# Kernel tuning notes

Hardware: AMD Instinct MI355X
Metric: run time of the kernel (lower is better)

## Reference

```python
import jax, jax.numpy as jnp
import numpy as np
from jax import lax

B, T, V, D, K = 64, 512, 32000, 768, 29

def setup_inputs() -> dict:
    key = jax.random.key(0)
    ks = jax.random.split(key, 8)
    x = jax.random.randint(ks[0], (B, T), 0, V)
    tags = jax.random.randint(ks[1], (B, T), 0, K)
    emb = jax.random.normal(ks[2], (V, D), dtype=jnp.float32) * 0.02
    w = jax.random.normal(ks[3], (K, D), dtype=jnp.float32) * 0.02
    b = jnp.zeros((K,), dtype=jnp.float32)
    start_trans = jax.random.normal(ks[4], (K,), dtype=jnp.float32) * 0.1
    end_trans = jax.random.normal(ks[5], (K,), dtype=jnp.float32) * 0.1
    trans = jax.random.normal(ks[6], (K, K), dtype=jnp.float32) * 0.1
    return {"x": x, "tags": tags, "emb": emb, "w": w, "b": b,
            "start_trans": start_trans, "end_trans": end_trans, "trans": trans}

def _emissions(x, emb, w, b):
    e = emb[x]                                   # [B,T,D] (dropout is identity at inference)
    return jnp.einsum('btd,kd->btk', e, w) + b   # [B,T,K]

def _crf_nll(em, tags, start_trans, end_trans, trans):
    # numerator: score of the gold tag path (full mask)
    num = start_trans[tags[:, 0]]
    num = num + jnp.take_along_axis(em[:, 0], tags[:, 0:1], axis=1)[:, 0]
    num = num + jnp.sum(trans[tags[:, :-1], tags[:, 1:]], axis=1)
    num = num + jnp.sum(jnp.take_along_axis(em[:, 1:], tags[:, 1:, None], axis=2)[..., 0], axis=1)
    num = num + end_trans[tags[:, -1]]
    # denominator: forward algorithm (log partition)
    def step(alpha, e_t):
        # alpha [B,K] prev-tag scores; e_t [B,K] current emissions
        nxt = jax.nn.logsumexp(alpha[:, :, None] + trans[None], axis=1) + e_t
        return nxt, None
    alpha0 = start_trans[None] + em[:, 0]
    alpha, _ = lax.scan(step, alpha0, jnp.swapaxes(em[:, 1:], 0, 1))
    logZ = jax.nn.logsumexp(alpha + end_trans[None], axis=1)
    return -jnp.sum(num - logZ)  # torchcrf default reduction='sum', model negates

def _viterbi(em, start_trans, end_trans, trans):
    def vstep(score, e_t):
        cand = score[:, :, None] + trans[None]   # [B,K_prev,K_cur]
        bp = jnp.argmax(cand, axis=1)            # [B,K]
        return jnp.max(cand, axis=1) + e_t, bp
    score0 = start_trans[None] + em[:, 0]
    score, bps = lax.scan(vstep, score0, jnp.swapaxes(em[:, 1:], 0, 1))  # bps [T-1,B,K]
    last = jnp.argmax(score + end_trans[None], axis=1)                   # [B]
    def back(tag, bp):
        prev = jnp.take_along_axis(bp, tag[:, None], axis=1)[:, 0]
        return prev, prev
    _, path = lax.scan(back, last, bps, reverse=True)                    # [T-1,B], tags 0..T-2
    return jnp.concatenate([jnp.swapaxes(path, 0, 1), last[:, None]], axis=1)

def reference(x, tags, emb, w, b, start_trans, end_trans, trans):
    em = _emissions(x, emb, w, b)
    nll = _crf_nll(em, tags, start_trans, end_trans, trans)
    decoded = _viterbi(em, start_trans, end_trans, trans)
    return nll, decoded
```

## Files before the change

kernel.cpp:

```cpp
#include <hip/hip_runtime.h>
#include <math.h>

#define NB 64
#define NT 512
#define ND 768
#define NK 29
#define L2E 1.4426950408889634f
#define LN2 0.6931471805599453f
#define NEG_BIG -1e30f

typedef __attribute__((ext_vector_type(8))) short short8;
typedef __attribute__((ext_vector_type(4))) float floatx4;

__device__ __forceinline__ short bf16r(float f) {
    unsigned u = __float_as_uint(f);
    unsigned r = (u + 0x7FFFu + ((u >> 16) & 1u)) >> 16;
    return (short)r;
}

__global__ __launch_bounds__(256) void k_prep(const float* __restrict__ w,
                                              short* __restrict__ wbf)
{
    int i = blockIdx.x * 256 + threadIdx.x;
    if (i < 32 * ND) {
        int row = i / ND;
        wbf[i] = (row < NK) ? bf16r(w[i]) : (short)0;
    }
}

__global__ __launch_bounds__(128, 2) void k_emissions(
    const int* __restrict__ x, const float* __restrict__ emb,
    const short* __restrict__ wbf, const float* __restrict__ bias,
    float* __restrict__ em)
{
    __shared__ float red[2 * 256];
    const int lane = threadIdx.x & 63;
    const int wv = threadIdx.x >> 6;
    const int col = lane & 15;
    const int quad = lane >> 4;
    const int Mbase = blockIdx.x * 16;
    const int tok = Mbase + col;

    const float* arow = emb + (size_t)x[tok] * ND + wv * 384 + quad * 8;
    const short* brow0 = wbf + (size_t)col * ND + wv * 384 + quad * 8;
    const short* brow1 = brow0 + 16 * ND;

    float4 a[24];
#pragma unroll
    for (int c = 0; c < 12; ++c) {
        a[2 * c]     = *(const float4*)(arow + c * 32);
        a[2 * c + 1] = *(const float4*)(arow + c * 32 + 4);
    }

    floatx4 acc0 = {0.f, 0.f, 0.f, 0.f};
    floatx4 acc1 = {0.f, 0.f, 0.f, 0.f};

    short8 b0 = *(const short8*)(brow0);
    short8 b1 = *(const short8*)(brow1);

#pragma unroll
    for (int c = 0; c < 12; ++c) {
        int c1 = (c + 1 <= 11) ? c + 1 : 11;
        short8 nb0 = *(const short8*)(brow0 + c1 * 32);
        short8 nb1 = *(const short8*)(brow1 + c1 * 32);

        short8 af;
        af[0] = bf16r(a[2 * c].x);     af[1] = bf16r(a[2 * c].y);
        af[2] = bf16r(a[2 * c].z);     af[3] = bf16r(a[2 * c].w);
        af[4] = bf16r(a[2 * c + 1].x); af[5] = bf16r(a[2 * c + 1].y);
        af[6] = bf16r(a[2 * c + 1].z); af[7] = bf16r(a[2 * c + 1].w);

        acc0 = __builtin_amdgcn_mfma_f32_16x16x32_bf16(af, b0, acc0, 0, 0, 0);
        acc1 = __builtin_amdgcn_mfma_f32_16x16x32_bf16(af, b1, acc1, 0, 0, 0);

        b0 = nb0; b1 = nb1;
    }

    const int r0 = quad * 4;
    if (wv == 1) {
#pragma unroll
        for (int reg = 0; reg < 4; ++reg) {
            red[(r0 + reg) * 16 + col]       = acc0[reg];
            red[256 + (r0 + reg) * 16 + col] = acc1[reg];
        }
    }
    __syncthreads();
    if (wv == 0) {
        float bs0 = bias[col];
        float bs1 = (col < NK - 16) ? bias[16 + col] : 0.f;
#pragma unroll
        for (int reg = 0; reg < 4; ++reg) {
            int row = r0 + reg;
            float v0 = acc0[reg] + red[row * 16 + col] + bs0;
            em[(size_t)(Mbase + row) * NK + col] = v0;
            if (col < NK - 16) {
                float v1 = acc1[reg] + red[256 + row * 16 + col] + bs1;
                em[(size_t)(Mbase + row) * NK + 16 + col] = v1;
            }
        }
    }
}

__global__ __launch_bounds__(64) void k_scan(
    const float* __restrict__ em, const int* __restrict__ tags,
    const float* __restrict__ st, const float* __restrict__ en,
    const float* __restrict__ tr, float* __restrict__ part,
    float* __restrict__ states)
{
    __shared__ __align__(16) float sA[32];
    __shared__ __align__(16) unsigned char smem[NT * NK * 4];
    const float4* sA4 = (const float4*)sA;
    const int lane = threadIdx.x;
    const int jc = (lane < NK) ? lane : NK - 1;

    if (blockIdx.x < NB) {
        const int b = blockIdx.x;
        float* emS = (float*)smem;
        {
            const float4* src = (const float4*)(em + (size_t)b * NT * NK);
            float4* dst = (float4*)emS;
            for (int i = lane; i < NT * NK / 4; i += 64) dst[i] = src[i];
        }
        float EC[32];
#pragma unroll
        for (int i = 0; i < NK; ++i) EC[i] = __expf(tr[i * NK + jc]);
#pragma unroll
        for (int i = NK; i < 32; ++i) EC[i] = 0.f;

        float a0v = __expf(st[jc] + emS[jc]);
        if (lane < 32) sA[lane] = (lane < NK) ? a0v : 0.f;

        int eshift = 5 * (NT - 1);
        float eemc = exp2f(fmaf(emS[NK + jc], L2E, -5.0f));
        float rawn = emS[2 * NK + jc];
        float anew = a0v;

        for (int t = 1; t < NT; ++t) {
            float4 A[8];
#pragma unroll
            for (int ii = 0; ii < 8; ++ii) A[ii] = sA4[ii];
            float p0 = 0.f, p1 = 0.f, p2 = 0.f, p3 = 0.f;
#pragma unroll
            for (int ii = 0; ii < 8; ++ii) {
                p0 = fmaf(A[ii].x, EC[4 * ii + 0], p0);
                p1 = fmaf(A[ii].y, EC[4 * ii + 1], p1);
                p2 = fmaf(A[ii].z, EC[4 * ii + 2], p2);
                p3 = fmaf(A[ii].w, EC[4 * ii + 3], p3);
            }
            anew = ((p0 + p1) + (p2 + p3)) * eemc;
            eemc = exp2f(fmaf(rawn, L2E, -5.0f));
            int tn = t + 2; tn = tn < NT ? tn : NT - 1;
            rawn = emS[tn * NK + jc];

            if ((t & 15) == 0) {
                unsigned mb = (unsigned)__builtin_amdgcn_readfirstlane(
                                  __float_as_int(anew));
                int ex = (int)((mb >> 23) & 255u) - 127;
                anew *= __int_as_float((unsigned)(127 - ex) << 23);
                eshift += ex;
            }
            if (lane < 32) sA[lane] = (lane < NK) ? anew : 0.f;
        }
        float val = (lane < NK) ? anew * __expf(en[jc]) : 0.f;
#pragma unroll
        for (int s = 32; s; s >>= 1) val += __shfl_xor(val, s);
        float logZ = logf(val) + (float)eshift * LN2;
        const int* tg = tags + b * NT;
        float p = 0.f;
        for (int t = lane; t < NT; t += 64) {
            int tt = tg[t];
            p += emS[t * NK + tt];
            if (t == 0) p += st[tt];
            else        p += tr[tg[t - 1] * NK + tt];
            if (t == NT - 1) p += en[tt];
        }
#pragma unroll
        for (int s = 32; s; s >>= 1) p += __shfl_xor(p, s);
        if (lane == 0) part[b] = logZ - p;
    } else {
        const int b = blockIdx.x - NB;
        const float* emb_b = em + (size_t)b * NT * NK;
        float* stt = states + (size_t)b * NT * 32;

        float Tc[32];
#pragma unroll
        for (int i = 0; i < NK; ++i) Tc[i] = tr[i * NK + jc];
#pragma unroll
        for (int i = NK; i < 32; ++i) Tc[i] = 0.f;

        float sc = (lane < NK) ? (st[jc] + emb_b[jc]) : NEG_BIG;
        if (lane < 32) { sA[lane] = sc; stt[lane] = sc; }

        float e0 = emb_b[1 * NK + jc];
        float e1 = emb_b[2 * NK + jc];
        float e2 = emb_b[3 * NK + jc];
        float e3 = emb_b[4 * NK + jc];

        auto vstep = [&](int t, float emt) {
            float4 q[8];
#pragma unroll
            for (int ii = 0; ii < 8; ++ii) q[ii] = sA4[ii];
            float v[32];
#pragma unroll
            for (int ii = 0; ii < 8; ++ii) {
                v[4 * ii + 0] = q[ii].x + Tc[4 * ii + 0];
                v[4 * ii + 1] = q[ii].y + Tc[4 * ii + 1];
                v[4 * ii + 2] = q[ii].z + Tc[4 * ii + 2];
                v[4 * ii + 3] = q[ii].w + Tc[4 * ii + 3];
            }
            float w0 = fmaxf(fmaxf(v[0], v[1]), v[2]);
            float w1 = fmaxf(fmaxf(v[3], v[4]), v[5]);
            float w2 = fmaxf(fmaxf(v[6], v[7]), v[8]);
            float w3 = fmaxf(fmaxf(v[9], v[10]), v[11]);
            float w4 = fmaxf(fmaxf(v[12], v[13]), v[14]);
            float w5 = fmaxf(fmaxf(v[15], v[16]), v[17]);
            float w6 = fmaxf(fmaxf(v[18], v[19]), v[20]);
            float w7 = fmaxf(fmaxf(v[21], v[22]), v[23]);
            float w8 = fmaxf(fmaxf(v[24], v[25]), v[26]);
            float w9 = fmaxf(fmaxf(v[27], v[28]), v[29]);
            float wa = fmaxf(v[30], v[31]);
            float u0 = fmaxf(fmaxf(w0, w1), w2);
            float u1 = fmaxf(fmaxf(w3, w4), w5);
            float u2 = fmaxf(fmaxf(w6, w7), w8);
            float u3 = fmaxf(w9, wa);
            float m  = fmaxf(fmaxf(fmaxf(u0, u1), u2), u3);

            sc = (lane < NK) ? (m + emt) : NEG_BIG;
            if (lane < 32) { sA[lane] = sc; stt[t * 32 + lane] = sc; }
        };

        int t = 1;
        for (; t + 3 < NT; t += 4) {
            vstep(t + 0, e0); { int tn = t + 4; tn = tn < NT ? tn : NT - 1; e0 = emb_b[tn * NK + jc]; }
            vstep(t + 1, e1); { int tn = t + 5; tn = tn < NT ? tn : NT - 1; e1 = emb_b[tn * NK + jc]; }
            vstep(t + 2, e2); { int tn = t + 6; tn = tn < NT ? tn : NT - 1; e2 = emb_b[tn * NK + jc]; }
            vstep(t + 3, e3); { int tn = t + 7; tn = tn < NT ? tn : NT - 1; e3 = emb_b[tn * NK + jc]; }
        }
        vstep(509, e0); vstep(510, e1); vstep(511, e2);
    }
}

__global__ __launch_bounds__(64) void k_bp(
    const float* __restrict__ states, const float* __restrict__ tr,
    unsigned char* __restrict__ bpg)
{
    __shared__ __align__(16) float stt[64 * 32];
    const int b = blockIdx.x >> 3;
    const int sg = blockIdx.x & 7;
    const int base = sg * 64;
    const float* S = states + (size_t)b * NT * 32 + (size_t)base * 32;
    const int tid = threadIdx.x;
    const int c = tid & 31;
    const int hw = tid >> 5;
    const int jc = (c < NK) ? c : NK - 1;

    float Tc[32];
#pragma unroll
    for (int i = 0; i < NK; ++i) Tc[i] = tr[i * NK + jc];
#pragma unroll
    for (int i = NK; i < 32; ++i) Tc[i] = 0.f;

    {
        const float4* src = (const float4*)S;
        float4* dst = (float4*)stt;
#pragma unroll
        for (int i = 0; i < 8; ++i) dst[tid + 64 * i] = src[tid + 64 * i];
    }
    __syncthreads();

    unsigned char* bpb = bpg + (size_t)b * 511 * 32;
#pragma unroll 1
    for (int k = 0; k < 32; ++k) {
        int rl = 2 * k + hw;
        int rr = base + rl;
        if (rr <= 510) {
            const float4* row = (const float4*)(stt + rl * 32);
            float4 q0 = row[0], q1 = row[1], q2 = row[2], q3 = row[3];
            float4 q4 = row[4], q5 = row[5], q6 = row[6], q7 = row[7];
            float v0  = q0.x + Tc[0],  v1  = q0.y + Tc[1];
            float v2  = q0.z + Tc[2],  v3  = q0.w + Tc[3];
            float v4  = q1.x + Tc[4],  v5  = q1.y + Tc[5];
            float v6  = q1.z + Tc[6],  v7  = q1.w + Tc[7];
            float v8  = q2.x + Tc[8],  v9  = q2.y + Tc[9];
            float v10 = q2.z + Tc[10], v11 = q2.w + Tc[11];
            float v12 = q3.x + Tc[12], v13 = q3.y + Tc[13];
            float v14 = q3.z + Tc[14], v15 = q3.w + Tc[15];
            float v16 = q4.x + Tc[16], v17 = q4.y + Tc[17];
            float v18 = q4.z + Tc[18], v19 = q4.w + Tc[19];
            float v20 = q5.x + Tc[20], v21 = q5.y + Tc[21];
            float v22 = q5.z + Tc[22], v23 = q5.w + Tc[23];
            float v24 = q6.x + Tc[24], v25 = q6.y + Tc[25];
            float v26 = q6.z + Tc[26], v27 = q6.w + Tc[27];
            float v28 = q7.x + Tc[28], v29 = q7.y + Tc[29];
            float v30 = q7.z + Tc[30], v31 = q7.w + Tc[31];
            float m0 = fmaxf(v0, v1),   m1 = fmaxf(v2, v3);
            float m2 = fmaxf(v4, v5),   m3 = fmaxf(v6, v7);
            float m4 = fmaxf(v8, v9),   m5 = fmaxf(v10, v11);
            float m6 = fmaxf(v12, v13), m7 = fmaxf(v14, v15);
            float m8 = fmaxf(v16, v17), m9 = fmaxf(v18, v19);
            float ma = fmaxf(v20, v21), mb = fmaxf(v22, v23);
            float mc = fmaxf(v24, v25), md = fmaxf(v26, v27);
            float me = fmaxf(v28, v29), mf = fmaxf(v30, v31);
            float n0 = fmaxf(m0, m1), n1 = fmaxf(m2, m3);
            float n2 = fmaxf(m4, m5), n3 = fmaxf(m6, m7);
            float n4 = fmaxf(m8, m9), n5 = fmaxf(ma, mb);
            float n6 = fmaxf(mc, md), n7 = fmaxf(me, mf);
            float o0 = fmaxf(n0, n1), o1 = fmaxf(n2, n3);
            float o2 = fmaxf(n4, n5), o3 = fmaxf(n6, n7);
            float m  = fmaxf(fmaxf(o0, o1), fmaxf(o2, o3));
            int idx = 31;
            idx = (v30 == m) ? 30 : idx;  idx = (v29 == m) ? 29 : idx;
            idx = (v28 == m) ? 28 : idx;  idx = (v27 == m) ? 27 : idx;
            idx = (v26 == m) ? 26 : idx;  idx = (v25 == m) ? 25 : idx;
            idx = (v24 == m) ? 24 : idx;  idx = (v23 == m) ? 23 : idx;
            idx = (v22 == m) ? 22 : idx;  idx = (v21 == m) ? 21 : idx;
            idx = (v20 == m) ? 20 : idx;  idx = (v19 == m) ? 19 : idx;
            idx = (v18 == m) ? 18 : idx;  idx = (v17 == m) ? 17 : idx;
            idx = (v16 == m) ? 16 : idx;  idx = (v15 == m) ? 15 : idx;
            idx = (v14 == m) ? 14 : idx;  idx = (v13 == m) ? 13 : idx;
            idx = (v12 == m) ? 12 : idx;  idx = (v11 == m) ? 11 : idx;
            idx = (v10 == m) ? 10 : idx;  idx = (v9  == m) ? 9  : idx;
            idx = (v8  == m) ? 8  : idx;  idx = (v7  == m) ? 7  : idx;
            idx = (v6  == m) ? 6  : idx;  idx = (v5  == m) ? 5  : idx;
            idx = (v4  == m) ? 4  : idx;  idx = (v3  == m) ? 3  : idx;
            idx = (v2  == m) ? 2  : idx;  idx = (v1  == m) ? 1  : idx;
            idx = (v0  == m) ? 0  : idx;
            bpb[(size_t)rr * 32 + c] = (unsigned char)idx;
        }
    }
}

__global__ __launch_bounds__(64) void k_trace(
    const unsigned char* __restrict__ bpg, const float* __restrict__ states,
    const float* __restrict__ en, float* __restrict__ out)
{
    __shared__ __align__(16) unsigned char sbp[511 * 32];
    __shared__ unsigned char smap[16 * 32];
    const int b = blockIdx.x;
    const int lane = threadIdx.x;
    const int jc = (lane < NK) ? lane : NK - 1;

    {
        const uint4* src = (const uint4*)(bpg + (size_t)b * 511 * 32);
        uint4* dst = (uint4*)sbp;
        for (int i = lane; i < 1022; i += 64) dst[i] = src[i];
    }
    __syncthreads();

    const float* fin = states + (size_t)b * NT * 32 + 511 * 32;
    int li = (lane < 32) ? lane : 0;
    float sv = fin[li];
    float vfin = (lane < NK) ? (sv + en[jc]) : NEG_BIG;
    float M = vfin;
#pragma unroll
    for (int s = 32; s; s >>= 1) M = fmaxf(M, __shfl_xor(M, s));
    unsigned long long mk = __ballot((lane < NK) && vfin == M);
    int last = (int)__builtin_ctzll(mk);

    const int cl = lane & 31;
    const int h = lane >> 5;
    int cur8[8];
#pragma unroll
    for (int rep = 0; rep < 8; ++rep) cur8[rep] = cl;
    for (int off = 0; off < 32; ++off) {
#pragma unroll
        for (int rep = 0; rep < 8; ++rep) {
            int s = 2 * rep + h;
            int hi = (s == 15) ? 511 : 32 * s + 32;
            int r = hi - 1 - off;
            if (r >= 32 * s) cur8[rep] = sbp[r * 32 + cur8[rep]];
        }
    }
#pragma unroll
    for (int rep = 0; rep < 8; ++rep)
        smap[(2 * rep + h) * 32 + cl] = (unsigned char)cur8[rep];

    int myhi = 0, cur = last;
    for (int s = 15; s >= 0; --s) {
        if (lane == s) myhi = cur;
        cur = smap[s * 32 + cur];
    }
    float* op = out + 1 + (size_t)b * NT;
    if (lane == 16) op[NT - 1] = (float)last;
    if (lane < 16) {
        int s = lane;
        int hi = (s == 15) ? 511 : 32 * s + 32;
        int cc = myhi;
        for (int r = hi - 1; r >= 32 * s; --r) {
            cc = sbp[r * 32 + cc];
            op[r] = (float)cc;
        }
    }
}

__global__ __launch_bounds__(64) void k_finish(const float* __restrict__ part,
                                               float* __restrict__ out)
{
    float v = part[threadIdx.x];
#pragma unroll
    for (int s = 32; s; s >>= 1) v += __shfl_xor(v, s);
    if (threadIdx.x == 0) out[0] = v;
}

extern "C" void kernel_launch(void* const* d_in, const int* in_sizes, int n_in,
                              void* d_out, int out_size, void* d_ws, size_t ws_size,
                              hipStream_t stream) {
    const int*   x    = (const int*)d_in[0];
    const int*   tags = (const int*)d_in[1];
    const float* emb  = (const float*)d_in[2];
    const float* w    = (const float*)d_in[3];
    const float* bias = (const float*)d_in[4];
    const float* st   = (const float*)d_in[5];
    const float* en   = (const float*)d_in[6];
    const float* tr   = (const float*)d_in[7];
    float* out = (float*)d_out;

    short* wbf    = (short*)d_ws;
    float* part   = (float*)((char*)d_ws + 49152);
    float* em     = (float*)((char*)d_ws + 65536);
    float* states = (float*)((char*)d_ws + 3932160);
    unsigned char* bp = (unsigned char*)((char*)d_ws + 65536);

    k_prep<<<96, 256, 0, stream>>>(w, wbf);
    k_emissions<<<2048, 128, 0, stream>>>(x, emb, wbf, bias, em);
    k_scan<<<2 * NB, 64, 0, stream>>>(em, tags, st, en, tr, part, states);
    k_bp<<<8 * NB, 64, 0, stream>>>(states, tr, bp);
    k_trace<<<NB, 64, 0, stream>>>(bp, states, en, out);
    k_finish<<<1, 64, 0, stream>>>(part, out);
}
```

Baseline: 314.8 us.

## Split scan reductions across wave halves and fuse backpointer, trace, finish kernels

The forward and Viterbi recurrences now use both 32-lane halves of the wave. Each half reduces over half of the previous tags, and the partial results are combined with a permlane32 swap, which shortens the serial per-step dependency chain. Separately, the backpointer, traceback and final-sum kernels are merged into one 512-thread block per sequence. Backpointers stay in LDS instead of being written to and reread from global memory, and two launches are removed. The trade-off is a large LDS footprint per block and fewer blocks for the backpointer computation.

Measured after the change: 288.2 us. 8.5% less time.

```diff
diff --git a/kernel.cpp b/kernel.cpp
--- a/kernel.cpp
+++ b/kernel.cpp
@@ -11,11 +11,19 @@
 
 typedef __attribute__((ext_vector_type(8))) short short8;
 typedef __attribute__((ext_vector_type(4))) float floatx4;
+typedef __attribute__((ext_vector_type(2))) unsigned u32x2;
 
 __device__ __forceinline__ short bf16r(float f) {
     unsigned u = __float_as_uint(f);
     unsigned r = (u + 0x7FFFu + ((u >> 16) & 1u)) >> 16;
     return (short)r;
+}
+
+__device__ __forceinline__ void swap32f(float x, float& a, float& b) {
+    u32x2 r = __builtin_amdgcn_permlane32_swap(__float_as_uint(x),
+                                               __float_as_uint(x), false, false);
+    a = __uint_as_float(r[0]);
+    b = __uint_as_float(r[1]);
 }
 
 __global__ __launch_bounds__(256) void k_prep(const float* __restrict__ w,
@@ -109,9 +117,10 @@
 {
     __shared__ __align__(16) float sA[32];
     __shared__ __align__(16) unsigned char smem[NT * NK * 4];
-    const float4* sA4 = (const float4*)sA;
     const int lane = threadIdx.x;
-    const int jc = (lane < NK) ? lane : NK - 1;
+    const int c = lane & 31;
+    const int h = lane >> 5;
+    const int jc = (c < NK) ? c : NK - 1;
 
     if (blockIdx.x < NB) {
         const int b = blockIdx.x;
@@ -121,11 +130,14 @@
             float4* dst = (float4*)emS;
             for (int i = lane; i < NT * NK / 4; i += 64) dst[i] = src[i];
         }
-        float EC[32];
-#pragma unroll
-        for (int i = 0; i < NK; ++i) EC[i] = __expf(tr[i * NK + jc]);
-#pragma unroll
-        for (int i = NK; i < 32; ++i) EC[i] = 0.f;
+        float EC0[8], EC1[8];
+#pragma unroll
+        for (int ii = 0; ii < 8; ++ii) {
+            int i0 = 4 * ii + 2 * h, i1 = i0 + 1;
+            EC0[ii] = (i0 < NK) ? __expf(tr[i0 * NK + jc]) : 0.f;
+            EC1[ii] = (i1 < NK) ? __expf(tr[i1 * NK + jc]) : 0.f;
+        }
+        const float2* sA2 = (const float2*)sA;
 
         float a0v = __expf(st[jc] + emS[jc]);
         if (lane < 32) sA[lane] = (lane < NK) ? a0v : 0.f;
@@ -136,18 +148,19 @@
         float anew = a0v;
 
         for (int t = 1; t < NT; ++t) {
-            float4 A[8];
-#pragma unroll
-            for (int ii = 0; ii < 8; ++ii) A[ii] = sA4[ii];
-            float p0 = 0.f, p1 = 0.f, p2 = 0.f, p3 = 0.f;
+            float2 q[8];
+#pragma unroll
+            for (int ii = 0; ii < 8; ++ii) q[ii] = sA2[2 * ii + h];
+            float ph0 = 0.f, ph1 = 0.f;
 #pragma unroll
             for (int ii = 0; ii < 8; ++ii) {
-                p0 = fmaf(A[ii].x, EC[4 * ii + 0], p0);
-                p1 = fmaf(A[ii].y, EC[4 * ii + 1], p1);
-                p2 = fmaf(A[ii].z, EC[4 * ii + 2], p2);
-                p3 = fmaf(A[ii].w, EC[4 * ii + 3], p3);
+                ph0 = fmaf(q[ii].x, EC0[ii], ph0);
+                ph1 = fmaf(q[ii].y, EC1[ii], ph1);
             }
-            anew = ((p0 + p1) + (p2 + p3)) * eemc;
+            float s = ph0 + ph1;
+            float r0, r1;
+            swap32f(s, r0, r1);
+            anew = (r0 + r1) * eemc;
             eemc = exp2f(fmaf(rawn, L2E, -5.0f));
             int tn = t + 2; tn = tn < NT ? tn : NT - 1;
             rawn = emS[tn * NK + jc];
@@ -182,11 +195,13 @@
         const float* emb_b = em + (size_t)b * NT * NK;
         float* stt = states + (size_t)b * NT * 32;
 
-        float Tc[32];
-#pragma unroll
-        for (int i = 0; i < NK; ++i) Tc[i] = tr[i * NK + jc];
-#pragma unroll
-        for (int i = NK; i < 32; ++i) Tc[i] = 0.f;
+        float Tch[16];
+#pragma unroll
+        for (int r = 0; r < 16; ++r) {
+            int i = 16 * h + r;
+            Tch[r] = (i < NK) ? tr[i * NK + jc] : 0.f;
+        }
+        const float4* sAh4 = (const float4*)(sA + 16 * h);
 
         float sc = (lane < NK) ? (st[jc] + emb_b[jc]) : NEG_BIG;
         if (lane < 32) { sA[lane] = sc; stt[lane] = sc; }
@@ -197,34 +212,25 @@
         float e3 = emb_b[4 * NK + jc];
 
         auto vstep = [&](int t, float emt) {
-            float4 q[8];
-#pragma unroll
-            for (int ii = 0; ii < 8; ++ii) q[ii] = sA4[ii];
-            float v[32];
-#pragma unroll
-            for (int ii = 0; ii < 8; ++ii) {
-                v[4 * ii + 0] = q[ii].x + Tc[4 * ii + 0];
-                v[4 * ii + 1] = q[ii].y + Tc[4 * ii + 1];
-                v[4 * ii + 2] = q[ii].z + Tc[4 * ii + 2];
-                v[4 * ii + 3] = q[ii].w + Tc[4 * ii + 3];
-            }
-            float w0 = fmaxf(fmaxf(v[0], v[1]), v[2]);
-            float w1 = fmaxf(fmaxf(v[3], v[4]), v[5]);
-            float w2 = fmaxf(fmaxf(v[6], v[7]), v[8]);
-            float w3 = fmaxf(fmaxf(v[9], v[10]), v[11]);
-            float w4 = fmaxf(fmaxf(v[12], v[13]), v[14]);
-            float w5 = fmaxf(fmaxf(v[15], v[16]), v[17]);
-            float w6 = fmaxf(fmaxf(v[18], v[19]), v[20]);
-            float w7 = fmaxf(fmaxf(v[21], v[22]), v[23]);
-            float w8 = fmaxf(fmaxf(v[24], v[25]), v[26]);
-            float w9 = fmaxf(fmaxf(v[27], v[28]), v[29]);
-            float wa = fmaxf(v[30], v[31]);
-            float u0 = fmaxf(fmaxf(w0, w1), w2);
-            float u1 = fmaxf(fmaxf(w3, w4), w5);
-            float u2 = fmaxf(fmaxf(w6, w7), w8);
-            float u3 = fmaxf(w9, wa);
-            float m  = fmaxf(fmaxf(fmaxf(u0, u1), u2), u3);
-
+            float4 q0 = sAh4[0], q1 = sAh4[1], q2 = sAh4[2], q3 = sAh4[3];
+            float v0  = q0.x + Tch[0],  v1  = q0.y + Tch[1];
+            float v2  = q0.z + Tch[2],  v3  = q0.w + Tch[3];
+            float v4  = q1.x + Tch[4],  v5  = q1.y + Tch[5];
+            float v6  = q1.z + Tch[6],  v7  = q1.w + Tch[7];
+            float v8  = q2.x + Tch[8],  v9  = q2.y + Tch[9];
+            float v10 = q2.z + Tch[10], v11 = q2.w + Tch[11];
+            float v12 = q3.x + Tch[12], v13 = q3.y + Tch[13];
+            float v14 = q3.z + Tch[14], v15 = q3.w + Tch[15];
+            float m0 = fmaxf(v0, v1),   m1 = fmaxf(v2, v3);
+            float m2 = fmaxf(v4, v5),   m3 = fmaxf(v6, v7);
+            float m4 = fmaxf(v8, v9),   m5 = fmaxf(v10, v11);
+            float m6 = fmaxf(v12, v13), m7 = fmaxf(v14, v15);
+            float n0 = fmaxf(m0, m1), n1 = fmaxf(m2, m3);
+            float n2 = fmaxf(m4, m5), n3 = fmaxf(m6, m7);
+            float mh = fmaxf(fmaxf(n0, n1), fmaxf(n2, n3));
+            float r0, r1;
+            swap32f(mh, r0, r1);
+            float m = fmaxf(r0, r1);
             sc = (lane < NK) ? (m + emt) : NEG_BIG;
             if (lane < 32) { sA[lane] = sc; stt[t * 32 + lane] = sc; }
         };
@@ -240,41 +246,40 @@
     }
 }
 
-__global__ __launch_bounds__(64) void k_bp(
+__global__ __launch_bounds__(512, 1) void k_post(
     const float* __restrict__ states, const float* __restrict__ tr,
-    unsigned char* __restrict__ bpg)
+    const float* __restrict__ en, const float* __restrict__ part,
+    float* __restrict__ out)
 {
-    __shared__ __align__(16) float stt[64 * 32];
-    const int b = blockIdx.x >> 3;
-    const int sg = blockIdx.x & 7;
-    const int base = sg * 64;
-    const float* S = states + (size_t)b * NT * 32 + (size_t)base * 32;
+    __shared__ __align__(16) float stt[NT * 32];
+    __shared__ __align__(16) unsigned char sbp[511 * 32];
+    __shared__ unsigned char smap[16 * 32];
+    const int b = blockIdx.x;
     const int tid = threadIdx.x;
     const int c = tid & 31;
-    const int hw = tid >> 5;
+    const int w = tid >> 5;
     const int jc = (c < NK) ? c : NK - 1;
 
+    {
+        const float4* src = (const float4*)(states + (size_t)b * NT * 32);
+        float4* dst = (float4*)stt;
+#pragma unroll
+        for (int i = 0; i < 8; ++i) dst[tid + 512 * i] = src[tid + 512 * i];
+    }
+
     float Tc[32];
 #pragma unroll
     for (int i = 0; i < NK; ++i) Tc[i] = tr[i * NK + jc];
 #pragma unroll
     for (int i = NK; i < 32; ++i) Tc[i] = 0.f;
 
-    {
-        const float4* src = (const float4*)S;
-        float4* dst = (float4*)stt;
-#pragma unroll
-        for (int i = 0; i < 8; ++i) dst[tid + 64 * i] = src[tid + 64 * i];
-    }
     __syncthreads();
 
-    unsigned char* bpb = bpg + (size_t)b * 511 * 32;
 #pragma unroll 1
     for (int k = 0; k < 32; ++k) {
-        int rl = 2 * k + hw;
-        int rr = base + rl;
+        int rr = 32 * w + k;
         if (rr <= 510) {
-            const float4* row = (const float4*)(stt + rl * 32);
+            const float4* row = (const float4*)(stt + rr * 32);
             float4 q0 = row[0], q1 = row[1], q2 = row[2], q3 = row[3];
             float4 q4 = row[4], q5 = row[5], q6 = row[6], q7 = row[7];
             float v0  = q0.x + Tc[0],  v1  = q0.y + Tc[1];
@@ -325,81 +330,62 @@
             idx = (v4  == m) ? 4  : idx;  idx = (v3  == m) ? 3  : idx;
             idx = (v2  == m) ? 2  : idx;  idx = (v1  == m) ? 1  : idx;
             idx = (v0  == m) ? 0  : idx;
-            bpb[(size_t)rr * 32 + c] = (unsigned char)idx;
-        }
-    }
-}
-
-__global__ __launch_bounds__(64) void k_trace(
-    const unsigned char* __restrict__ bpg, const float* __restrict__ states,
-    const float* __restrict__ en, float* __restrict__ out)
-{
-    __shared__ __align__(16) unsigned char sbp[511 * 32];
-    __shared__ unsigned char smap[16 * 32];
-    const int b = blockIdx.x;
-    const int lane = threadIdx.x;
-    const int jc = (lane < NK) ? lane : NK - 1;
-
-    {
-        const uint4* src = (const uint4*)(bpg + (size_t)b * 511 * 32);
-        uint4* dst = (uint4*)sbp;
-        for (int i = lane; i < 1022; i += 64) dst[i] = src[i];
+            sbp[rr * 32 + c] = (unsigned char)idx;
+        }
     }
     __syncthreads();
 
-    const float* fin = states + (size_t)b * NT * 32 + 511 * 32;
-    int li = (lane < 32) ? lane : 0;
-    float sv = fin[li];
-    float vfin = (lane < NK) ? (sv + en[jc]) : NEG_BIG;
-    float M = vfin;
-#pragma unroll
-    for (int s = 32; s; s >>= 1) M = fmaxf(M, __shfl_xor(M, s));
-    unsigned long long mk = __ballot((lane < NK) && vfin == M);
-    int last = (int)__builtin_ctzll(mk);
-
-    const int cl = lane & 31;
-    const int h = lane >> 5;
-    int cur8[8];
-#pragma unroll
-    for (int rep = 0; rep < 8; ++rep) cur8[rep] = cl;
-    for (int off = 0; off < 32; ++off) {
-#pragma unroll
-        for (int rep = 0; rep < 8; ++rep) {
-            int s = 2 * rep + h;
+    if (tid < 64) {
+        const int lane = tid;
+        float sv = stt[511 * 32 + ((lane < 32) ? lane : 0)];
+        float vfin = (lane < NK) ? (sv + en[jc]) : NEG_BIG;
+        float M = vfin;
+#pragma unroll
+        for (int s = 32; s; s >>= 1) M = fmaxf(M, __shfl_xor(M, s));
+        unsigned long long mk = __ballot((lane < NK) && vfin == M);
+        int last = (int)__builtin_ctzll(mk);
+
+        const int cl = lane & 31;
+        const int hh = lane >> 5;
+        int cur8[8];
+#pragma unroll
+        for (int rep = 0; rep < 8; ++rep) cur8[rep] = cl;
+        for (int off = 0; off < 32; ++off) {
+#pragma unroll
+            for (int rep = 0; rep < 8; ++rep) {
+                int s = 2 * rep + hh;
+                int hi = (s == 15) ? 511 : 32 * s + 32;
+                int r = hi - 1 - off;
+                if (r >= 32 * s) cur8[rep] = sbp[r * 32 + cur8[rep]];
+            }
+        }
+#pragma unroll
+        for (int rep = 0; rep < 8; ++rep)
+            smap[(2 * rep + hh) * 32 + cl] = (unsigned char)cur8[rep];
+
+        int myhi = 0, cur = last;
+        for (int s = 15; s >= 0; --s) {
+            if (lane == s) myhi = cur;
+            cur = smap[s * 32 + cur];
+        }
+        float* op = out + 1 + (size_t)b * NT;
+        if (lane == 16) op[NT - 1] = (float)last;
+        if (lane < 16) {
+            int s = lane;
             int hi = (s == 15) ? 511 : 32 * s + 32;
-            int r = hi - 1 - off;
-            if (r >= 32 * s) cur8[rep] = sbp[r * 32 + cur8[rep]];
-        }
-    }
-#pragma unroll
-    for (int rep = 0; rep < 8; ++rep)
-        smap[(2 * rep + h) * 32 + cl] = (unsigned char)cur8[rep];
-
-    int myhi = 0, cur = last;
-    for (int s = 15; s >= 0; --s) {
-        if (lane == s) myhi = cur;
-        cur = smap[s * 32 + cur];
-    }
-    float* op = out + 1 + (size_t)b * NT;
-    if (lane == 16) op[NT - 1] = (float)last;
-    if (lane < 16) {
-        int s = lane;
-        int hi = (s == 15) ? 511 : 32 * s + 32;
-        int cc = myhi;
-        for (int r = hi - 1; r >= 32 * s; --r) {
-            cc = sbp[r * 32 + cc];
-            op[r] = (float)cc;
-        }
-    }
-}
-
-__global__ __launch_bounds__(64) void k_finish(const float* __restrict__ part,
-                                               float* __restrict__ out)
-{
-    float v = part[threadIdx.x];
-#pragma unroll
-    for (int s = 32; s; s >>= 1) v += __shfl_xor(v, s);
-    if (threadIdx.x == 0) out[0] = v;
+            int cc = myhi;
+            for (int r = hi - 1; r >= 32 * s; --r) {
+                cc = sbp[r * 32 + cc];
+                op[r] = (float)cc;
+            }
+        }
+    } else if (b == 0 && tid < 128) {
+        int l2 = tid - 64;
+        float v = part[l2];
+#pragma unroll
+        for (int s = 32; s; s >>= 1) v += __shfl_xor(v, s);
+        if (l2 == 0) out[0] = v;
+    }
 }
 
 extern "C" void kernel_launch(void* const* d_in, const int* in_sizes, int n_in,
@@ -419,12 +405,9 @@
     float* part   = (float*)((char*)d_ws + 49152);
     float* em     = (float*)((char*)d_ws + 65536);
     float* states = (float*)((char*)d_ws + 3932160);
-    unsigned char* bp = (unsigned char*)((char*)d_ws + 65536);
 
     k_prep<<<96, 256, 0, stream>>>(w, wbf);
     k_emissions<<<2048, 128, 0, stream>>>(x, emb, wbf, bias, em);
     k_scan<<<2 * NB, 64, 0, stream>>>(em, tags, st, en, tr, part, states);
-    k_bp<<<8 * NB, 64, 0, stream>>>(states, tr, bp);
-    k_trace<<<NB, 64, 0, stream>>>(bp, states, en, out);
-    k_finish<<<1, 64, 0, stream>>>(part, out);
-}
+    k_post<<<NB, 512, 0, stream>>>(states, tr, en, part, out);
+}
```
